# Performance work log

Hardware: AMD Instinct MI355X
Metric: run time of the kernel (lower is better)

## Reference

```python
import jax, jax.numpy as jnp
import numpy as np

TOP_K = 4
N_GROUP = 8
TOPK_GROUP = 4
SCALE = 1.0

B, S, H, I, E = 2, 1024, 1024, 512, 32
SHARED_I = I * 2  # n_shared_experts = 2


def setup_inputs() -> dict:
    key = jax.random.key(0)
    ks = jax.random.split(key, 9)
    return {
        "hidden_states": jax.random.normal(ks[0], (B, S, H), jnp.float32),
        "gate_w": jax.random.normal(ks[1], (E, H), jnp.float32) * 0.02,
        "gate_bias": jnp.zeros((E,), jnp.float32),
        "gate_proj": jax.random.normal(ks[2], (E, I, H), jnp.float32) * 0.02,
        "up_proj": jax.random.normal(ks[3], (E, I, H), jnp.float32) * 0.02,
        "down_proj": jax.random.normal(ks[4], (E, H, I), jnp.float32) * 0.02,
        "shared_gate_w": jax.random.normal(ks[5], (SHARED_I, H), jnp.float32) * 0.02,
        "shared_up_w": jax.random.normal(ks[6], (SHARED_I, H), jnp.float32) * 0.02,
        "shared_down_w": jax.random.normal(ks[7], (H, SHARED_I), jnp.float32) * 0.02,
    }


def reference(hidden_states, gate_w, gate_bias, gate_proj, up_proj, down_proj,
              shared_gate_w, shared_up_w, shared_down_w):
    b, s, h = hidden_states.shape
    e = gate_w.shape[0]
    x = hidden_states.reshape(-1, h)            # (T, H)
    t = x.shape[0]

    # ---- gating (DeepSeek-V3 grouped sigmoid routing) ----
    logits = x @ gate_w.T                       # (T, E)
    scores = jax.nn.sigmoid(logits)
    sfc = scores + gate_bias[None, :]           # scores_for_choice
    # per-group score = sum of top-2 experts in group
    group_scores = jax.lax.top_k(sfc.reshape(t, N_GROUP, -1), 2)[0].sum(-1)  # (T, G)
    _, gidx = jax.lax.top_k(group_scores, TOPK_GROUP)                        # (T, topk_group)
    gmask = jax.nn.one_hot(gidx, N_GROUP, dtype=sfc.dtype).sum(1)            # (T, G)
    smask = jnp.repeat(gmask, e // N_GROUP, axis=1)                          # (T, E)
    tmp = jnp.where(smask > 0, sfc, 0.0)
    _, topk_idx = jax.lax.top_k(tmp, TOP_K)                                  # (T, K)
    topk_w = jnp.take_along_axis(scores, topk_idx, axis=1)                   # (T, K)
    topk_w = topk_w / (topk_w.sum(-1, keepdims=True) + 1e-20)                # norm_topk_prob
    topk_w = topk_w * SCALE

    # ---- routed experts (dense combine-weight formulation) ----
    comb = jnp.zeros((t, e), x.dtype).at[jnp.arange(t)[:, None], topk_idx].add(topk_w)  # (T, E)
    g = jnp.einsum('th,eih->eti', x, gate_proj)   # (E, T, I)
    u = jnp.einsum('th,eih->eti', x, up_proj)     # (E, T, I)
    a = jax.nn.silu(g) * u
    a = a * comb.T[:, :, None]                    # scale before down-proj to skip zero experts
    out = jnp.einsum('eti,ehi->th', a, down_proj) # (T, H)

    # ---- shared experts ----
    sg = x @ shared_gate_w.T
    su = x @ shared_up_w.T
    out = out + (jax.nn.silu(sg) * su) @ shared_down_w.T

    return out.reshape(b, s, h)
```

## Files before the change

### kernel.cpp

```cpp
#include <hip/hip_runtime.h>
#include <hip/hip_bf16.h>
#include <cstdint>
#include <cstddef>

#define H_DIM 1024
#define I_DIM 512
#define E_NUM 32
#define SHARED_I_DIM 1024
#define TOPK 4
#define NGROUP 8
#define TOPKG 4
#define GT 8

typedef __attribute__((ext_vector_type(8))) short bf16x8;
typedef __attribute__((ext_vector_type(4))) float f32x4;
typedef __attribute__((ext_vector_type(8))) unsigned short u16x8;

__device__ inline unsigned short f2bf(float f) {
    __hip_bfloat16 h = __float2bfloat16(f);
    return *reinterpret_cast<unsigned short*>(&h);
}
__device__ inline float bf2f(unsigned short u) {
    union { unsigned int u; float f; } w;
    w.u = ((unsigned int)u) << 16;
    return w.f;
}

__device__ inline void bar_lds() {
    asm volatile("s_waitcnt lgkmcnt(0)" ::: "memory");
    __builtin_amdgcn_s_barrier();
}

__device__ inline int laddr(int row, int chunk) {
    return row * 64 + ((chunk ^ (row & 7)) << 3);
}

__global__ void init_kernel(int* cnt) {
    if (threadIdx.x < 64) cnt[threadIdx.x] = 0;
}

__global__ void cvt_kernel(const float* __restrict__ src, unsigned short* __restrict__ dst, int n8) {
    int i = blockIdx.x * blockDim.x + threadIdx.x;
    if (i >= n8) return;
    float4 a = *(const float4*)(src + (size_t)i * 8);
    float4 b = *(const float4*)(src + (size_t)i * 8 + 4);
    u16x8 v;
    v[0] = f2bf(a.x); v[1] = f2bf(a.y); v[2] = f2bf(a.z); v[3] = f2bf(a.w);
    v[4] = f2bf(b.x); v[5] = f2bf(b.y); v[6] = f2bf(b.z); v[7] = f2bf(b.w);
    *(u16x8*)(dst + (size_t)i * 8) = v;
}

__global__ __launch_bounds__(256) void gate_kernel(const float* __restrict__ x,
                                                   const float* __restrict__ gw,
                                                   float* __restrict__ logits_out) {
    int tb = blockIdx.x;
    int tid = threadIdx.x;
    __shared__ float xs[GT][H_DIM];
    __shared__ float ps[8][GT][E_NUM];
    const float* xsrc = x + (size_t)tb * GT * H_DIM;
    for (int i = tid; i < GT * H_DIM / 4; i += 256)
        ((float4*)&xs[0][0])[i] = ((const float4*)xsrc)[i];
    __syncthreads();
    int e = tid & 31, part = tid >> 5;
    const float* wrow = gw + (size_t)e * H_DIM + part * 128;
    float acc[GT] = {};
    for (int c0 = 0; c0 < 128; c0 += 32) {
        float w[32];
#pragma unroll
        for (int c = 0; c < 32; c++) w[c] = wrow[c0 + c];
#pragma unroll
        for (int t = 0; t < GT; t++) {
#pragma unroll
            for (int c = 0; c < 32; c++)
                acc[t] += w[c] * xs[t][part * 128 + c0 + c];
        }
    }
#pragma unroll
    for (int t = 0; t < GT; t++) ps[part][t][e] = acc[t];
    __syncthreads();
    {
        int t = tid >> 5, ee = tid & 31;
        float s = 0.f;
#pragma unroll
        for (int p = 0; p < 8; p++) s += ps[p][t][ee];
        logits_out[((size_t)tb * GT + t) * E_NUM + ee] = s;
    }
}

__global__ void select_kernel(const float* __restrict__ logits, const float* __restrict__ gb,
                              int* __restrict__ topk_e, float* __restrict__ topk_w,
                              int* __restrict__ cnt, int T) {
    int t = blockIdx.x * blockDim.x + threadIdx.x;
    if (t >= T) return;
    float scores[E_NUM], sfc[E_NUM];
#pragma unroll
    for (int i = 0; i < E_NUM; i++) {
        float l = logits[(size_t)t * E_NUM + i];
        float s = 1.f / (1.f + expf(-l));
        scores[i] = s;
        sfc[i] = s + gb[i];
    }
    float gs[NGROUP];
#pragma unroll
    for (int g = 0; g < NGROUP; g++) {
        float m1 = -1e30f, m2 = -1e30f;
#pragma unroll
        for (int j = 0; j < 4; j++) {
            float v = sfc[g * 4 + j];
            if (v > m1) { m2 = m1; m1 = v; }
            else if (v > m2) { m2 = v; }
        }
        gs[g] = m1 + m2;
    }
    unsigned gmask = 0;
    for (int r = 0; r < TOPKG; r++) {
        int best = 0; float bv = -1e30f;
#pragma unroll
        for (int g = 0; g < NGROUP; g++)
            if (!((gmask >> g) & 1u) && gs[g] > bv) { bv = gs[g]; best = g; }
        gmask |= 1u << best;
    }
    unsigned cmask = 0;
    int eidx[TOPK]; float ew[TOPK]; float sum = 0.f;
    for (int r = 0; r < TOPK; r++) {
        int best = 0; float bv = -1e30f; float bsc = 0.f;
#pragma unroll
        for (int i = 0; i < E_NUM; i++) {
            float v = ((gmask >> (i >> 2)) & 1u) ? sfc[i] : 0.0f;
            if (!((cmask >> i) & 1u) && v > bv) { bv = v; best = i; bsc = scores[i]; }
        }
        cmask |= 1u << best;
        eidx[r] = best; ew[r] = bsc; sum += bsc;
    }
    float inv = 1.f / (sum + 1e-20f);
#pragma unroll
    for (int k = 0; k < TOPK; k++) {
        topk_e[t * TOPK + k] = eidx[k];
        topk_w[t * TOPK + k] = ew[k] * inv;
        atomicAdd(&cnt[eidx[k]], 1);
    }
}

__global__ void scan_kernel(const int* __restrict__ cnt, int* __restrict__ off) {
    if (threadIdx.x == 0) {
        int a = 0;
        for (int e = 0; e < E_NUM; e++) { off[e] = a; a += cnt[e]; }
        off[E_NUM] = a;
    }
}

__global__ void bin_kernel(const int* __restrict__ topk_e, const float* __restrict__ topk_w,
                           const int* __restrict__ off, int* __restrict__ cnt2,
                           int* __restrict__ slot_token, float* __restrict__ slot_w,
                           int* __restrict__ slot_of, int total) {
    int i = blockIdx.x * blockDim.x + threadIdx.x;
    if (i >= total) return;
    int e = topk_e[i];
    float w = topk_w[i];
    int pos = atomicAdd(&cnt2[e], 1);
    int slot = off[e] + pos;
    slot_token[slot] = i >> 2;
    slot_w[slot] = w;
    slot_of[i] = slot;
}

__global__ __launch_bounds__(256) void combine_kernel(const unsigned short* __restrict__ out_slot,
                                                      const int* __restrict__ slot_of,
                                                      float* __restrict__ out) {
    int t = blockIdx.x;
    int h = threadIdx.x * 4;
    int s0 = slot_of[t * TOPK + 0], s1 = slot_of[t * TOPK + 1];
    int s2 = slot_of[t * TOPK + 2], s3 = slot_of[t * TOPK + 3];
    ushort4 a = *(const ushort4*)(out_slot + (size_t)s0 * H_DIM + h);
    ushort4 b = *(const ushort4*)(out_slot + (size_t)s1 * H_DIM + h);
    ushort4 c = *(const ushort4*)(out_slot + (size_t)s2 * H_DIM + h);
    ushort4 d = *(const ushort4*)(out_slot + (size_t)s3 * H_DIM + h);
    float4 o = *(float4*)(out + (size_t)t * H_DIM + h);
    o.x += bf2f(a.x) + bf2f(b.x) + bf2f(c.x) + bf2f(d.x);
    o.y += bf2f(a.y) + bf2f(b.y) + bf2f(c.y) + bf2f(d.y);
    o.z += bf2f(a.z) + bf2f(b.z) + bf2f(c.z) + bf2f(d.z);
    o.w += bf2f(a.w) + bf2f(b.w) + bf2f(c.w) + bf2f(d.w);
    *(float4*)(out + (size_t)t * H_DIM + h) = o;
}

template <int MODE, bool DUAL, int BM, bool ROUTED, bool AGATHER>
__global__ __launch_bounds__(512, 2) void gemm_kernel(
    const unsigned short* __restrict__ A, const float* __restrict__ B1,
    const float* __restrict__ B2, size_t bstride,
    void* __restrict__ Dst, int ldD,
    const int* __restrict__ slot_token, const float* __restrict__ slot_w,
    const int* __restrict__ cnt, const int* __restrict__ off_arr, int K, int Mtot) {
    static_assert(MODE != 0 || DUAL, "MODE0 requires DUAL");
    constexpr int RW = BM / 4;
    constexpr int MF = RW / 16;
    constexpr int ACH = BM / 64;
    constexpr int TPR = 512 / BM;

    int itile, mtile, e;
    if constexpr (ROUTED) { e = blockIdx.x; itile = blockIdx.y; mtile = blockIdx.z; }
    else                  { itile = blockIdx.x; mtile = blockIdx.y; e = 0; }
    int count = Mtot, base = 0;
    if (ROUTED) {
        count = cnt[e];
        base = off_arr[e];
        if (mtile * BM >= count) return;
    }

    __shared__ __align__(16) unsigned short As[2][BM * 64];
    __shared__ __align__(16) unsigned short Bs1[2][64 * 64];
    __shared__ __align__(16) unsigned short Bs2[2][DUAL ? 64 * 64 : 8];

    int tid = threadIdx.x;

    int as_row = tid / TPR;
    int as_cb = (tid % TPR) * ACH;
    int am = mtile * BM + as_row;
    int ar;
    if (AGATHER)      ar = (am < count) ? slot_token[base + am] : 0;
    else if (ROUTED)  ar = base + ((am < count) ? am : 0);
    else              ar = (am < count) ? am : 0;
    const unsigned short* Arow = A + (size_t)ar * K + as_cb * 8;

    int bs_row = tid >> 3, bs_ch = tid & 7;
    const float* B1r = B1 + (size_t)e * bstride + (size_t)(itile * 64 + bs_row) * K + bs_ch * 8;
    const float* B2r = DUAL ? (B2 + (size_t)e * bstride + (size_t)(itile * 64 + bs_row) * K + bs_ch * 8)
                            : nullptr;

    f32x4 acc1[MF][2] = {};
    f32x4 acc2[DUAL ? MF : 1][2] = {};

    int lane = tid & 63, wid = tid >> 6;
    int wrow = (wid >> 1) * RW, wcol = (wid & 1) * 32;
    int frow = lane & 15, fch = lane >> 4;

    u16x8 pA0[ACH], pA1[ACH];
    float4 b1lo0, b1hi0, b1lo1, b1hi1;
    float4 b2lo0, b2hi0, b2lo1, b2hi1;

    auto loadS = [&](u16x8* pA, float4& b1lo, float4& b1hi, float4& b2lo, float4& b2hi, int k0) {
#pragma unroll
        for (int c = 0; c < ACH; c++) pA[c] = *(const u16x8*)(Arow + k0 + c * 8);
        b1lo = *(const float4*)(B1r + k0);
        b1hi = *(const float4*)(B1r + k0 + 4);
        if constexpr (DUAL) {
            b2lo = *(const float4*)(B2r + k0);
            b2hi = *(const float4*)(B2r + k0 + 4);
        }
    };
    auto writeS = [&](int buf, const u16x8* pA, float4 b1lo, float4 b1hi, float4 b2lo, float4 b2hi) {
        unsigned short* As_ = As[buf];
        unsigned short* Bs1_ = Bs1[buf];
#pragma unroll
        for (int c = 0; c < ACH; c++)
            *(u16x8*)(&As_[laddr(as_row, as_cb + c)]) = pA[c];
        u16x8 s;
        s[0] = f2bf(b1lo.x); s[1] = f2bf(b1lo.y); s[2] = f2bf(b1lo.z); s[3] = f2bf(b1lo.w);
        s[4] = f2bf(b1hi.x); s[5] = f2bf(b1hi.y); s[6] = f2bf(b1hi.z); s[7] = f2bf(b1hi.w);
        *(u16x8*)(&Bs1_[laddr(bs_row, bs_ch)]) = s;
        if constexpr (DUAL) {
            unsigned short* Bs2_ = Bs2[buf];
            u16x8 s2;
            s2[0] = f2bf(b2lo.x); s2[1] = f2bf(b2lo.y); s2[2] = f2bf(b2lo.z); s2[3] = f2bf(b2lo.w);
            s2[4] = f2bf(b2hi.x); s2[5] = f2bf(b2hi.y); s2[6] = f2bf(b2hi.z); s2[7] = f2bf(b2hi.w);
            *(u16x8*)(&Bs2_[laddr(bs_row, bs_ch)]) = s2;
        }
    };
    auto compute = [&](int buf) {
        const unsigned short* As_ = As[buf];
        const unsigned short* Bs1_ = Bs1[buf];
        const unsigned short* Bs2_ = Bs2[buf];
#pragma unroll
        for (int kk = 0; kk < 2; kk++) {
            int cb = fch + kk * 4;
            bf16x8 bf1[2], bf2[DUAL ? 2 : 1], af[MF];
#pragma unroll
            for (int nf = 0; nf < 2; nf++)
                bf1[nf] = *(const bf16x8*)(&Bs1_[laddr(wcol + nf * 16 + frow, cb)]);
            if constexpr (DUAL) {
#pragma unroll
                for (int nf = 0; nf < 2; nf++)
                    bf2[nf] = *(const bf16x8*)(&Bs2_[laddr(wcol + nf * 16 + frow, cb)]);
            }
#pragma unroll
            for (int mf = 0; mf < MF; mf++)
                af[mf] = *(const bf16x8*)(&As_[laddr(wrow + mf * 16 + frow, cb)]);
#pragma unroll
            for (int mf = 0; mf < MF; mf++)
#pragma unroll
                for (int nf = 0; nf < 2; nf++) {
                    acc1[mf][nf] = __builtin_amdgcn_mfma_f32_16x16x32_bf16(af[mf], bf1[nf], acc1[mf][nf], 0, 0, 0);
                    if constexpr (DUAL)
                        acc2[mf][nf] = __builtin_amdgcn_mfma_f32_16x16x32_bf16(af[mf], bf2[nf], acc2[mf][nf], 0, 0, 0);
                }
        }
    };

    const int NK = K >> 6;
    loadS(pA0, b1lo0, b1hi0, b2lo0, b2hi0, 0);
    loadS(pA1, b1lo1, b1hi1, b2lo1, b2hi1, 64);
    writeS(0, pA0, b1lo0, b1hi0, b2lo0, b2hi0);
    loadS(pA0, b1lo0, b1hi0, b2lo0, b2hi0, 128);
    bar_lds();
    for (int it = 0; it < NK; it += 2) {
        writeS(1, pA1, b1lo1, b1hi1, b2lo1, b2hi1);
        if (it + 3 < NK) loadS(pA1, b1lo1, b1hi1, b2lo1, b2hi1, (it + 3) << 6);
        compute(0);
        bar_lds();
        if (it + 2 < NK) {
            writeS(0, pA0, b1lo0, b1hi0, b2lo0, b2hi0);
            if (it + 4 < NK) loadS(pA0, b1lo0, b1hi0, b2lo0, b2hi0, (it + 4) << 6);
        }
        compute(1);
        if (it + 2 < NK) bar_lds();
    }

#pragma unroll
    for (int mf = 0; mf < MF; mf++)
#pragma unroll
        for (int nf = 0; nf < 2; nf++)
#pragma unroll
            for (int j = 0; j < 4; j++) {
                int rloc = wrow + mf * 16 + (lane >> 4) * 4 + j;
                int mrow = mtile * BM + rloc;
                int col = itile * 64 + wcol + nf * 16 + (lane & 15);
                if (mrow >= count) continue;
                if constexpr (MODE == 0) {
                    float w = ROUTED ? slot_w[base + mrow] : 1.0f;
                    float g = acc1[mf][nf][j];
                    float a = (g / (1.f + __expf(-g))) * acc2[mf][nf][j] * w;
                    ((unsigned short*)Dst)[(size_t)(base + mrow) * ldD + col] = f2bf(a);
                } else if constexpr (MODE == 1) {
                    ((float*)Dst)[(size_t)mrow * ldD + col] = acc1[mf][nf][j];
                } else {
                    ((unsigned short*)Dst)[(size_t)(base + mrow) * ldD + col] = f2bf(acc1[mf][nf][j]);
                }
            }
}

extern "C" void kernel_launch(void* const* d_in, const int* in_sizes, int n_in,
                              void* d_out, int out_size, void* d_ws, size_t ws_size,
                              hipStream_t stream) {
    const float* x = (const float*)d_in[0];
    const float* gw = (const float*)d_in[1];
    const float* gb = (const float*)d_in[2];
    const float* gate_proj = (const float*)d_in[3];
    const float* up_proj = (const float*)d_in[4];
    const float* down_proj = (const float*)d_in[5];
    const float* sgw = (const float*)d_in[6];
    const float* suw = (const float*)d_in[7];
    const float* sdw = (const float*)d_in[8];
    float* out = (float*)d_out;

    const int T = in_sizes[0] / H_DIM;
    const int total_slots = T * TOPK;

    char* ws = (char*)d_ws;
    int* cnt = (int*)ws;
    int* cnt2 = cnt + 32;
    int* off = cnt + 64;
    int* topk_e = cnt + 128;
    float* topk_w = (float*)(topk_e + total_slots);
    int* slot_token = (int*)(topk_w + total_slots);
    float* slot_w = (float*)(slot_token + total_slots);
    int* slot_of = (int*)(slot_w + total_slots);
    float* logits = (float*)(slot_of + total_slots);
    unsigned short* x_bf = (unsigned short*)(logits + (size_t)T * E_NUM);
    unsigned short* act_r = x_bf + (size_t)T * H_DIM;
    unsigned short* act_s = act_r + (size_t)(total_slots + 256) * I_DIM;
    unsigned short* out_slot = act_s + (size_t)T * SHARED_I_DIM;

    hipLaunchKernelGGL(init_kernel, dim3(1), dim3(64), 0, stream, cnt);
    hipLaunchKernelGGL(cvt_kernel, dim3((T * H_DIM / 8 + 255) / 256), dim3(256), 0, stream,
                       x, x_bf, T * H_DIM / 8);
    hipLaunchKernelGGL(gate_kernel, dim3(T / GT), dim3(256), 0, stream, x, gw, logits);
    hipLaunchKernelGGL(select_kernel, dim3((T + 255) / 256), dim3(256), 0, stream,
                       logits, gb, topk_e, topk_w, cnt, T);
    hipLaunchKernelGGL(scan_kernel, dim3(1), dim3(1), 0, stream, cnt, off);
    hipLaunchKernelGGL(bin_kernel, dim3((total_slots + 255) / 256), dim3(256), 0, stream,
                       topk_e, topk_w, off, cnt2, slot_token, slot_w, slot_of, total_slots);

    hipLaunchKernelGGL((gemm_kernel<0, true, 256, true, true>),
                       dim3(E_NUM, I_DIM / 64, 32), dim3(512), 0, stream,
                       x_bf, gate_proj, up_proj, (size_t)I_DIM * H_DIM,
                       (void*)act_r, I_DIM, slot_token, slot_w, cnt, off, H_DIM, 0);

    hipLaunchKernelGGL((gemm_kernel<0, true, 128, false, false>),
                       dim3(SHARED_I_DIM / 64, T / 128, 1), dim3(512), 0, stream,
                       x_bf, sgw, suw, (size_t)0,
                       (void*)act_s, SHARED_I_DIM, (const int*)nullptr, (const float*)nullptr,
                       (const int*)nullptr, (const int*)nullptr, H_DIM, T);

    hipLaunchKernelGGL((gemm_kernel<1, false, 128, false, false>),
                       dim3(H_DIM / 64, T / 128, 1), dim3(512), 0, stream,
                       act_s, sdw, (const float*)nullptr, (size_t)0,
                       (void*)out, H_DIM, (const int*)nullptr, (const float*)nullptr,
                       (const int*)nullptr, (const int*)nullptr, SHARED_I_DIM, T);

    hipLaunchKernelGGL((gemm_kernel<3, false, 256, true, false>),
                       dim3(E_NUM, H_DIM / 64, 32), dim3(512), 0, stream,
                       act_r, down_proj, (const float*)nullptr, (size_t)H_DIM * I_DIM,
                       (void*)out_slot, H_DIM, slot_token, (const float*)nullptr, cnt, off, I_DIM, 0);

    hipLaunchKernelGGL(combine_kernel, dim3(T), dim3(256), 0, stream, out_slot, slot_of, out);
}
```

Before: 206.6 us.

## Merge routed and shared expert GEMMs into two fused launches with K=32 tiles

Replaces four separate GEMM launches with two: stage one computes the routed gate/up projections and the shared gate/up projections in a single grid, using an extra expert index for the shared expert. Stage two does the same for the down projections. The LDS tile shrinks from K=64 to K=32 and the weight loading is split so each half of the block loads one of the two B matrices. The shared-expert M tile grows from 128 to 256. The aim is to cut launch count and fill the GPU better by letting shared and routed work run concurrently, at the cost of more K iterations and barriers per tile.

New measurement: 211.7 us. 2.5% more time.

```diff
diff --git a/kernel.cpp b/kernel.cpp
--- a/kernel.cpp
+++ b/kernel.cpp
@@ -31,8 +31,8 @@
     __builtin_amdgcn_s_barrier();
 }
 
-__device__ inline int laddr(int row, int chunk) {
-    return row * 64 + ((chunk ^ (row & 7)) << 3);
+__device__ inline int laddr32(int row, int chunk) {
+    return row * 32 + (((chunk) ^ (row & 3)) << 3);
 }
 
 __global__ void init_kernel(int* cnt) {
@@ -183,156 +183,144 @@
     *(float4*)(out + (size_t)t * H_DIM + h) = o;
 }
 
-template <int MODE, bool DUAL, int BM, bool ROUTED, bool AGATHER>
-__global__ __launch_bounds__(512, 2) void gemm_kernel(
-    const unsigned short* __restrict__ A, const float* __restrict__ B1,
-    const float* __restrict__ B2, size_t bstride,
-    void* __restrict__ Dst, int ldD,
+template <bool STAGE1>
+__global__ __launch_bounds__(512, 2) void moe_gemm(
+    const unsigned short* __restrict__ Axr, const unsigned short* __restrict__ Axs,
+    const float* __restrict__ B1r_, const float* __restrict__ B2r_,
+    const float* __restrict__ B1s_, const float* __restrict__ B2s_,
+    void* __restrict__ Dr, void* __restrict__ Ds,
     const int* __restrict__ slot_token, const float* __restrict__ slot_w,
-    const int* __restrict__ cnt, const int* __restrict__ off_arr, int K, int Mtot) {
-    static_assert(MODE != 0 || DUAL, "MODE0 requires DUAL");
-    constexpr int RW = BM / 4;
-    constexpr int MF = RW / 16;
-    constexpr int ACH = BM / 64;
-    constexpr int TPR = 512 / BM;
-
-    int itile, mtile, e;
-    if constexpr (ROUTED) { e = blockIdx.x; itile = blockIdx.y; mtile = blockIdx.z; }
-    else                  { itile = blockIdx.x; mtile = blockIdx.y; e = 0; }
-    int count = Mtot, base = 0;
-    if (ROUTED) {
-        count = cnt[e];
-        base = off_arr[e];
-        if (mtile * BM >= count) return;
-    }
-
-    __shared__ __align__(16) unsigned short As[2][BM * 64];
-    __shared__ __align__(16) unsigned short Bs1[2][64 * 64];
-    __shared__ __align__(16) unsigned short Bs2[2][DUAL ? 64 * 64 : 8];
+    const int* __restrict__ cnt, const int* __restrict__ off_arr, int T) {
+    constexpr bool DUAL = STAGE1;
+    int e = blockIdx.x, itile = blockIdx.y, mtile = blockIdx.z;
+    bool sh = (e == E_NUM);
+    int NI = (STAGE1 && !sh) ? (I_DIM / 64) : 16;
+    if (itile >= NI) return;
+    int count = sh ? T : cnt[e];
+    int base = sh ? 0 : off_arr[e];
+    if (mtile * 256 >= count) return;
+    const int K = STAGE1 ? H_DIM : (sh ? SHARED_I_DIM : I_DIM);
+
+    __shared__ __align__(16) unsigned short LA[2][256 * 32];
+    __shared__ __align__(16) unsigned short LB1[2][64 * 32];
+    __shared__ __align__(16) unsigned short LB2[2][DUAL ? 64 * 32 : 8];
 
     int tid = threadIdx.x;
-
-    int as_row = tid / TPR;
-    int as_cb = (tid % TPR) * ACH;
-    int am = mtile * BM + as_row;
-    int ar;
-    if (AGATHER)      ar = (am < count) ? slot_token[base + am] : 0;
-    else if (ROUTED)  ar = base + ((am < count) ? am : 0);
-    else              ar = (am < count) ? am : 0;
-    const unsigned short* Arow = A + (size_t)ar * K + as_cb * 8;
-
-    int bs_row = tid >> 3, bs_ch = tid & 7;
-    const float* B1r = B1 + (size_t)e * bstride + (size_t)(itile * 64 + bs_row) * K + bs_ch * 8;
-    const float* B2r = DUAL ? (B2 + (size_t)e * bstride + (size_t)(itile * 64 + bs_row) * K + bs_ch * 8)
-                            : nullptr;
-
-    f32x4 acc1[MF][2] = {};
-    f32x4 acc2[DUAL ? MF : 1][2] = {};
+    int as_row = tid >> 1, asub = tid & 1;
+    int am = mtile * 256 + as_row;
+    int amc = (am < count) ? am : 0;
+    const unsigned short* Arow;
+    if constexpr (STAGE1) {
+        int tok = sh ? amc : slot_token[base + amc];
+        Arow = Axr + (size_t)tok * H_DIM + asub * 16;
+    } else {
+        Arow = sh ? (Axs + (size_t)amc * SHARED_I_DIM + asub * 16)
+                  : (Axr + (size_t)(base + amc) * I_DIM + asub * 16);
+    }
+    int half = tid >> 8;
+    int bt = tid & 255;
+    int b_row = bt >> 2, b_ch = bt & 3;
+    int brow = itile * 64 + b_row;
+    const float* Bsrc;
+    if constexpr (STAGE1) {
+        if (sh) Bsrc = (half ? B2s_ : B1s_) + (size_t)brow * K + b_ch * 8;
+        else    Bsrc = (half ? B2r_ : B1r_) + (size_t)e * (I_DIM * H_DIM) + (size_t)brow * K + b_ch * 8;
+    } else {
+        Bsrc = sh ? (B1s_ + (size_t)brow * K + b_ch * 8)
+                  : (B1r_ + (size_t)e * (H_DIM * I_DIM) + (size_t)brow * K + b_ch * 8);
+    }
+    const bool doB = DUAL || (half == 0);
+
+    f32x4 acc1[4][2] = {};
+    f32x4 acc2[DUAL ? 4 : 1][2] = {};
 
     int lane = tid & 63, wid = tid >> 6;
-    int wrow = (wid >> 1) * RW, wcol = (wid & 1) * 32;
+    int wrow = (wid >> 1) * 64, wcol = (wid & 1) * 32;
     int frow = lane & 15, fch = lane >> 4;
 
-    u16x8 pA0[ACH], pA1[ACH];
-    float4 b1lo0, b1hi0, b1lo1, b1hi1;
-    float4 b2lo0, b2hi0, b2lo1, b2hi1;
-
-    auto loadS = [&](u16x8* pA, float4& b1lo, float4& b1hi, float4& b2lo, float4& b2hi, int k0) {
-#pragma unroll
-        for (int c = 0; c < ACH; c++) pA[c] = *(const u16x8*)(Arow + k0 + c * 8);
-        b1lo = *(const float4*)(B1r + k0);
-        b1hi = *(const float4*)(B1r + k0 + 4);
-        if constexpr (DUAL) {
-            b2lo = *(const float4*)(B2r + k0);
-            b2hi = *(const float4*)(B2r + k0 + 4);
+    u16x8 pA0[2], pA1[2];
+    float4 blo0, bhi0, blo1, bhi1;
+
+    auto loadS = [&](u16x8* pA, float4& blo, float4& bhi, int k0) {
+        pA[0] = *(const u16x8*)(Arow + k0);
+        pA[1] = *(const u16x8*)(Arow + k0 + 8);
+        if (doB) {
+            blo = *(const float4*)(Bsrc + k0);
+            bhi = *(const float4*)(Bsrc + k0 + 4);
         }
     };
-    auto writeS = [&](int buf, const u16x8* pA, float4 b1lo, float4 b1hi, float4 b2lo, float4 b2hi) {
-        unsigned short* As_ = As[buf];
-        unsigned short* Bs1_ = Bs1[buf];
-#pragma unroll
-        for (int c = 0; c < ACH; c++)
-            *(u16x8*)(&As_[laddr(as_row, as_cb + c)]) = pA[c];
-        u16x8 s;
-        s[0] = f2bf(b1lo.x); s[1] = f2bf(b1lo.y); s[2] = f2bf(b1lo.z); s[3] = f2bf(b1lo.w);
-        s[4] = f2bf(b1hi.x); s[5] = f2bf(b1hi.y); s[6] = f2bf(b1hi.z); s[7] = f2bf(b1hi.w);
-        *(u16x8*)(&Bs1_[laddr(bs_row, bs_ch)]) = s;
-        if constexpr (DUAL) {
-            unsigned short* Bs2_ = Bs2[buf];
-            u16x8 s2;
-            s2[0] = f2bf(b2lo.x); s2[1] = f2bf(b2lo.y); s2[2] = f2bf(b2lo.z); s2[3] = f2bf(b2lo.w);
-            s2[4] = f2bf(b2hi.x); s2[5] = f2bf(b2hi.y); s2[6] = f2bf(b2hi.z); s2[7] = f2bf(b2hi.w);
-            *(u16x8*)(&Bs2_[laddr(bs_row, bs_ch)]) = s2;
+    auto writeS = [&](int buf, const u16x8* pA, float4 blo, float4 bhi) {
+        *(u16x8*)(&LA[buf][laddr32(as_row, asub * 2)]) = pA[0];
+        *(u16x8*)(&LA[buf][laddr32(as_row, asub * 2 + 1)]) = pA[1];
+        if (doB) {
+            u16x8 s;
+            s[0] = f2bf(blo.x); s[1] = f2bf(blo.y); s[2] = f2bf(blo.z); s[3] = f2bf(blo.w);
+            s[4] = f2bf(bhi.x); s[5] = f2bf(bhi.y); s[6] = f2bf(bhi.z); s[7] = f2bf(bhi.w);
+            unsigned short* d = (DUAL && half) ? &LB2[buf][0] : &LB1[buf][0];
+            *(u16x8*)(&d[laddr32(b_row, b_ch)]) = s;
         }
     };
     auto compute = [&](int buf) {
-        const unsigned short* As_ = As[buf];
-        const unsigned short* Bs1_ = Bs1[buf];
-        const unsigned short* Bs2_ = Bs2[buf];
-#pragma unroll
-        for (int kk = 0; kk < 2; kk++) {
-            int cb = fch + kk * 4;
-            bf16x8 bf1[2], bf2[DUAL ? 2 : 1], af[MF];
+        bf16x8 af[4], bf1[2], bf2[DUAL ? 2 : 1];
+#pragma unroll
+        for (int nf = 0; nf < 2; nf++)
+            bf1[nf] = *(const bf16x8*)(&LB1[buf][laddr32(wcol + nf * 16 + frow, fch)]);
+        if constexpr (DUAL) {
 #pragma unroll
             for (int nf = 0; nf < 2; nf++)
-                bf1[nf] = *(const bf16x8*)(&Bs1_[laddr(wcol + nf * 16 + frow, cb)]);
-            if constexpr (DUAL) {
-#pragma unroll
-                for (int nf = 0; nf < 2; nf++)
-                    bf2[nf] = *(const bf16x8*)(&Bs2_[laddr(wcol + nf * 16 + frow, cb)]);
+                bf2[nf] = *(const bf16x8*)(&LB2[buf][laddr32(wcol + nf * 16 + frow, fch)]);
+        }
+#pragma unroll
+        for (int mf = 0; mf < 4; mf++)
+            af[mf] = *(const bf16x8*)(&LA[buf][laddr32(wrow + mf * 16 + frow, fch)]);
+#pragma unroll
+        for (int mf = 0; mf < 4; mf++)
+#pragma unroll
+            for (int nf = 0; nf < 2; nf++) {
+                acc1[mf][nf] = __builtin_amdgcn_mfma_f32_16x16x32_bf16(af[mf], bf1[nf], acc1[mf][nf], 0, 0, 0);
+                if constexpr (DUAL)
+                    acc2[mf][nf] = __builtin_amdgcn_mfma_f32_16x16x32_bf16(af[mf], bf2[nf], acc2[mf][nf], 0, 0, 0);
             }
-#pragma unroll
-            for (int mf = 0; mf < MF; mf++)
-                af[mf] = *(const bf16x8*)(&As_[laddr(wrow + mf * 16 + frow, cb)]);
-#pragma unroll
-            for (int mf = 0; mf < MF; mf++)
-#pragma unroll
-                for (int nf = 0; nf < 2; nf++) {
-                    acc1[mf][nf] = __builtin_amdgcn_mfma_f32_16x16x32_bf16(af[mf], bf1[nf], acc1[mf][nf], 0, 0, 0);
-                    if constexpr (DUAL)
-                        acc2[mf][nf] = __builtin_amdgcn_mfma_f32_16x16x32_bf16(af[mf], bf2[nf], acc2[mf][nf], 0, 0, 0);
-                }
-        }
     };
 
-    const int NK = K >> 6;
-    loadS(pA0, b1lo0, b1hi0, b2lo0, b2hi0, 0);
-    loadS(pA1, b1lo1, b1hi1, b2lo1, b2hi1, 64);
-    writeS(0, pA0, b1lo0, b1hi0, b2lo0, b2hi0);
-    loadS(pA0, b1lo0, b1hi0, b2lo0, b2hi0, 128);
+    const int NK = K >> 5;
+    loadS(pA0, blo0, bhi0, 0);
+    loadS(pA1, blo1, bhi1, 32);
+    writeS(0, pA0, blo0, bhi0);
+    loadS(pA0, blo0, bhi0, 64);
     bar_lds();
     for (int it = 0; it < NK; it += 2) {
-        writeS(1, pA1, b1lo1, b1hi1, b2lo1, b2hi1);
-        if (it + 3 < NK) loadS(pA1, b1lo1, b1hi1, b2lo1, b2hi1, (it + 3) << 6);
+        writeS(1, pA1, blo1, bhi1);
+        if (it + 3 < NK) loadS(pA1, blo1, bhi1, (it + 3) << 5);
         compute(0);
         bar_lds();
         if (it + 2 < NK) {
-            writeS(0, pA0, b1lo0, b1hi0, b2lo0, b2hi0);
-            if (it + 4 < NK) loadS(pA0, b1lo0, b1hi0, b2lo0, b2hi0, (it + 4) << 6);
+            writeS(0, pA0, blo0, bhi0);
+            if (it + 4 < NK) loadS(pA0, blo0, bhi0, (it + 4) << 5);
         }
         compute(1);
         if (it + 2 < NK) bar_lds();
     }
 
 #pragma unroll
-    for (int mf = 0; mf < MF; mf++)
+    for (int mf = 0; mf < 4; mf++)
 #pragma unroll
         for (int nf = 0; nf < 2; nf++)
 #pragma unroll
             for (int j = 0; j < 4; j++) {
                 int rloc = wrow + mf * 16 + (lane >> 4) * 4 + j;
-                int mrow = mtile * BM + rloc;
+                int mrow = mtile * 256 + rloc;
                 int col = itile * 64 + wcol + nf * 16 + (lane & 15);
                 if (mrow >= count) continue;
-                if constexpr (MODE == 0) {
-                    float w = ROUTED ? slot_w[base + mrow] : 1.0f;
+                if constexpr (STAGE1) {
+                    float w = sh ? 1.0f : slot_w[base + mrow];
                     float g = acc1[mf][nf][j];
                     float a = (g / (1.f + __expf(-g))) * acc2[mf][nf][j] * w;
-                    ((unsigned short*)Dst)[(size_t)(base + mrow) * ldD + col] = f2bf(a);
-                } else if constexpr (MODE == 1) {
-                    ((float*)Dst)[(size_t)mrow * ldD + col] = acc1[mf][nf][j];
+                    if (sh) ((unsigned short*)Ds)[(size_t)mrow * SHARED_I_DIM + col] = f2bf(a);
+                    else    ((unsigned short*)Dr)[(size_t)(base + mrow) * I_DIM + col] = f2bf(a);
                 } else {
-                    ((unsigned short*)Dst)[(size_t)(base + mrow) * ldD + col] = f2bf(acc1[mf][nf][j]);
+                    if (sh) ((float*)Ds)[(size_t)mrow * H_DIM + col] = acc1[mf][nf][j];
+                    else    ((unsigned short*)Dr)[(size_t)(base + mrow) * H_DIM + col] = f2bf(acc1[mf][nf][j]);
                 }
             }
 }
@@ -379,27 +367,17 @@
     hipLaunchKernelGGL(bin_kernel, dim3((total_slots + 255) / 256), dim3(256), 0, stream,
                        topk_e, topk_w, off, cnt2, slot_token, slot_w, slot_of, total_slots);
 
-    hipLaunchKernelGGL((gemm_kernel<0, true, 256, true, true>),
-                       dim3(E_NUM, I_DIM / 64, 32), dim3(512), 0, stream,
-                       x_bf, gate_proj, up_proj, (size_t)I_DIM * H_DIM,
-                       (void*)act_r, I_DIM, slot_token, slot_w, cnt, off, H_DIM, 0);
-
-    hipLaunchKernelGGL((gemm_kernel<0, true, 128, false, false>),
-                       dim3(SHARED_I_DIM / 64, T / 128, 1), dim3(512), 0, stream,
-                       x_bf, sgw, suw, (size_t)0,
-                       (void*)act_s, SHARED_I_DIM, (const int*)nullptr, (const float*)nullptr,
-                       (const int*)nullptr, (const int*)nullptr, H_DIM, T);
-
-    hipLaunchKernelGGL((gemm_kernel<1, false, 128, false, false>),
-                       dim3(H_DIM / 64, T / 128, 1), dim3(512), 0, stream,
-                       act_s, sdw, (const float*)nullptr, (size_t)0,
-                       (void*)out, H_DIM, (const int*)nullptr, (const float*)nullptr,
-                       (const int*)nullptr, (const int*)nullptr, SHARED_I_DIM, T);
-
-    hipLaunchKernelGGL((gemm_kernel<3, false, 256, true, false>),
-                       dim3(E_NUM, H_DIM / 64, 32), dim3(512), 0, stream,
-                       act_r, down_proj, (const float*)nullptr, (size_t)H_DIM * I_DIM,
-                       (void*)out_slot, H_DIM, slot_token, (const float*)nullptr, cnt, off, I_DIM, 0);
+    hipLaunchKernelGGL((moe_gemm<true>), dim3(E_NUM + 1, 16, 16), dim3(512), 0, stream,
+                       x_bf, (const unsigned short*)nullptr,
+                       gate_proj, up_proj, sgw, suw,
+                       (void*)act_r, (void*)act_s,
+                       slot_token, slot_w, cnt, off, T);
+
+    hipLaunchKernelGGL((moe_gemm<false>), dim3(E_NUM + 1, 16, 16), dim3(512), 0, stream,
+                       act_r, act_s,
+                       down_proj, (const float*)nullptr, sdw, (const float*)nullptr,
+                       (void*)out_slot, (void*)out,
+                       slot_token, slot_w, cnt, off, T);
 
     hipLaunchKernelGGL(combine_kernel, dim3(T), dim3(256), 0, stream, out_slot, slot_of, out);
 }
```
